# Kernel tuning notes

Hardware: AMD Instinct MI355X
Metric: run time of the kernel (lower is better)

The kernel has to match this reference:

```python
import jax, jax.numpy as jnp
import numpy as np

EPS = 1e-5
K = 5          # kernel size from SE3Convolution(5, ...)
STRIDE = 2
PAD = 3
C_HID = 52     # 4*dim(repr3x3=9) + dim(repr7=7) + dim(repr9=9)
N_CLASSES = 10


def conv3d(x, w):
    # x: [N, Cin, D, H, W], w: [Cout, Cin, K, K, K]
    return jax.lax.conv_general_dilated(
        x, w,
        window_strides=(STRIDE, STRIDE, STRIDE),
        padding=[(PAD, PAD)] * 3,
        dimension_numbers=("NCDHW", "OIDHW", "NCDHW"),
    )


def bn3d(x):
    # training-mode batch norm over (batch, spatial), per channel, no affine
    mean = jnp.mean(x, axis=(0, 2, 3, 4), keepdims=True)
    var = jnp.var(x, axis=(0, 2, 3, 4), keepdims=True)
    return (x - mean) * jax.lax.rsqrt(var + EPS)


def setup_inputs() -> dict:
    key = jax.random.key(0)
    ks = jax.random.split(key, 10)
    x = jax.random.normal(ks[0], (32, 1, 64, 64, 64), dtype=jnp.float32)
    s = 0.05
    w0 = jax.random.normal(ks[1], (C_HID, 1, K, K, K), jnp.float32) * s
    b0 = jax.random.normal(ks[2], (C_HID,), jnp.float32) * s
    w1 = jax.random.normal(ks[3], (C_HID, C_HID, K, K, K), jnp.float32) * s
    b1 = jax.random.normal(ks[4], (C_HID,), jnp.float32) * s
    w2 = jax.random.normal(ks[5], (C_HID, C_HID, K, K, K), jnp.float32) * s
    b2 = jax.random.normal(ks[6], (C_HID,), jnp.float32) * s
    w3 = jax.random.normal(ks[7], (N_CLASSES, C_HID, K, K, K), jnp.float32) * s
    gamma = jnp.ones((N_CLASSES,), jnp.float32)
    beta = jnp.zeros((N_CLASSES,), jnp.float32)
    return {"x": x, "w0": w0, "b0": b0, "w1": w1, "b1": b1,
            "w2": w2, "b2": b2, "w3": w3, "gamma": gamma, "beta": beta}


def reference(x, w0, b0, w1, b1, w2, b2, w3, gamma, beta):
    # bn_in: BatchNorm3d(1, affine=False)
    h = bn3d(x)
    # three conv blocks with scalar batch norm + bias + ReLU (non_lin layers)
    for w, b in ((w0, b0), (w1, b1), (w2, b2)):
        h = conv3d(h, w)
        h = bn3d(h)
        h = jax.nn.relu(h + b[None, :, None, None, None])
    # final conv (no nonlinearity)
    h = conv3d(h, w3)
    # global average pool over x, y, z -> [batch, classes]
    h = jnp.mean(h, axis=(2, 3, 4))
    # bn_out: affine batch norm over the batch dim, per class
    mean = jnp.mean(h, axis=0, keepdims=True)
    var = jnp.var(h, axis=0, keepdims=True)
    h = (h - mean) * jax.lax.rsqrt(var + EPS)
    return h * gamma[None, :] + beta[None, :]
```

## Files before the change

### kernel.cpp

```cpp
#include <hip/hip_runtime.h>
#include <hip/hip_bf16.h>

#define EPSV 1e-5f
constexpr int NB = 32;

typedef short bf16x8 __attribute__((ext_vector_type(8)));
typedef short short4v __attribute__((ext_vector_type(4)));
typedef float f32x4 __attribute__((ext_vector_type(4)));

__device__ inline float bf2f(short s) {
  return __uint_as_float(((unsigned)(unsigned short)s) << 16);
}
__device__ inline short f2bf(float f) {
  unsigned u = __float_as_uint(f);
  unsigned r = (u + 0x7FFFu + ((u >> 16) & 1u)) >> 16;
  return (short)r;
}

__global__ __launch_bounds__(256) void reduce_partial_f32(
    const float* __restrict__ in, int spatial, float* __restrict__ part,
    int totb, int boff)
{
  const int b = blockIdx.x;
  const int nblk = gridDim.x;
  float s = 0.f, s2 = 0.f;
  for (int n = 0; n < NB; ++n) {
    const float* p = in + (size_t)n * spatial;
    for (int i = b * 256 + threadIdx.x; i < spatial; i += nblk * 256) {
      float v = p[i];
      s += v; s2 += v * v;
    }
  }
  __shared__ float sh[256], sh2[256];
  int tid = threadIdx.x;
  sh[tid] = s; sh2[tid] = s2;
  __syncthreads();
  for (int off = 128; off > 0; off >>= 1) {
    if (tid < off) { sh[tid] += sh[tid + off]; sh2[tid] += sh2[tid + off]; }
    __syncthreads();
  }
  if (tid == 0) {
    part[(size_t)(boff + b) * 2 + 0] = sh[0];
    part[(size_t)(boff + b) * 2 + 1] = sh2[0];
  }
}

__global__ __launch_bounds__(256) void reduce_cl(
    const short* __restrict__ y, long nrows,
    float* __restrict__ part, int totb, int boff)
{
  const int b = blockIdx.x, nblk = gridDim.x;
  const int c = threadIdx.x & 63, seg = threadIdx.x >> 6;
  float s = 0.f, s2 = 0.f;
  for (long r = (long)b * 4 + seg; r < nrows; r += (long)nblk * 4) {
    float v = bf2f(y[r * 64 + c]);
    s += v; s2 += v * v;
  }
  __shared__ float sh[4][64], sh2[4][64];
  sh[seg][c] = s; sh2[seg][c] = s2;
  __syncthreads();
  if (seg == 0) {
    float a = sh[0][c] + sh[1][c] + sh[2][c] + sh[3][c];
    float a2 = sh2[0][c] + sh2[1][c] + sh2[2][c] + sh2[3][c];
    part[((size_t)c * totb + boff + b) * 2 + 0] = a;
    part[((size_t)c * totb + boff + b) * 2 + 1] = a2;
  }
}

__global__ __launch_bounds__(64) void reduce_final(
    const float* __restrict__ part, int nblk, int C, float* __restrict__ sums)
{
  const int c = blockIdx.x;
  float s = 0.f, s2 = 0.f;
  for (int b = threadIdx.x; b < nblk; b += 64) {
    s  += part[((size_t)c * nblk + b) * 2 + 0];
    s2 += part[((size_t)c * nblk + b) * 2 + 1];
  }
  for (int off = 32; off > 0; off >>= 1) {
    s  += __shfl_down(s, off);
    s2 += __shfl_down(s2, off);
  }
  if (threadIdx.x == 0) { sums[c] = s; sums[C + c] = s2; }
}

__global__ __launch_bounds__(64) void aff_k(
    const float* __restrict__ st, const float* __restrict__ bias,
    float cnt_inv, int creal, float* __restrict__ a, float* __restrict__ c)
{
  int t = threadIdx.x;
  float mean = st[t] * cnt_inv;
  float var  = st[64 + t] * cnt_inv - mean * mean;
  float inv  = rsqrtf(var + EPSV);
  bool ok = t < creal;
  a[t] = ok ? inv : 0.f;
  c[t] = ok ? (-mean * inv + bias[t]) : 0.f;
}

__global__ __launch_bounds__(256) void repack_k(
    const float* __restrict__ w, short* __restrict__ wt,
    int CO, int CIN, int COP)
{
  long total = 125L * COP * 64;
  for (long idx = (long)blockIdx.x * 256 + threadIdx.x; idx < total;
       idx += (long)gridDim.x * 256) {
    int tap = (int)(idx / (COP * 64));
    int r   = (int)(idx % (COP * 64));
    int co = r >> 6, ci = r & 63;
    float v = (co < CO && ci < CIN) ? w[((size_t)co * CIN + ci) * 125 + tap] : 0.f;
    wt[idx] = f2bf(v);
  }
}

__global__ __launch_bounds__(256) void repack_w0(
    const float* __restrict__ w, short* __restrict__ wt)
{
  for (int idx = blockIdx.x * 256 + threadIdx.x; idx < 64 * 128;
       idx += gridDim.x * 256) {
    int co = idx >> 7, k = idx & 127;
    float v = (co < 52 && k < 125) ? w[co * 125 + k] : 0.f;
    wt[idx] = f2bf(v);
  }
}

__global__ __launch_bounds__(256) void conv0_mfma(
    const float* __restrict__ x, const short* __restrict__ w0t,
    const float* __restrict__ stats, short* __restrict__ out,
    int n_in0, int n_out0)
{
  constexpr int IN = 64, OUT = 33;
  constexpr float CNTI = 1.0f / ((float)NB * IN * IN * IN);
  __shared__ __align__(16) char slab[64 * 256];

  const int tid = threadIdx.x;
  const int wv = tid >> 6, ln = tid & 63;
  const int cs = ln >> 4;
  const int ntile0 = blockIdx.x * 64;
  const int od = blockIdx.y;
  const int img = blockIdx.z;

  const float mean = stats[0] * CNTI;
  const float inv  = rsqrtf(stats[1] * CNTI - mean * mean + EPSV);

  bf16x8 afr[4];
  {
    const short* wrow = w0t + (wv * 16 + (ln & 15)) * 128 + cs * 8;
    #pragma unroll
    for (int ks = 0; ks < 4; ++ks) afr[ks] = *(const bf16x8*)(wrow + ks * 32);
  }

  const float* xi = x + (size_t)(n_in0 + img) * (IN * IN * IN);
  const int id_base = 2 * od - 3;
  for (int u = tid; u < 1024; u += 256) {
    const int nl = u >> 4, s = u & 15;
    const int ng = ntile0 + nl;
    const int oh = ng / OUT, ow = ng - oh * OUT;
    const bool nok = ng < OUT * OUT;
    const int ih_base = 2 * oh - 3, iw_base = 2 * ow - 3;
    bf16x8 pk;
    #pragma unroll
    for (int e = 0; e < 8; ++e) {
      const int k = s * 8 + e;
      float f = 0.f;
      if (nok && k < 125) {
        const int kd = k / 25, r = k - kd * 25;
        const int kh = r / 5, kw = r - kh * 5;
        const int id = id_base + kd, ih = ih_base + kh, iw = iw_base + kw;
        if ((unsigned)id < (unsigned)IN && (unsigned)ih < (unsigned)IN &&
            (unsigned)iw < (unsigned)IN)
          f = (xi[((size_t)id * IN + ih) * IN + iw] - mean) * inv;
      }
      pk[e] = f2bf(f);
    }
    const int slot = (s & 8) | ((s & 7) ^ (nl & 7));
    *(bf16x8*)(slab + nl * 256 + slot * 16) = pk;
  }
  __syncthreads();

  const int nl = ln & 15;
  #pragma unroll
  for (int nt = 0; nt < 4; ++nt) {
    f32x4 acc = (f32x4){0.f, 0.f, 0.f, 0.f};
    const int nn = nt * 16 + nl;
    #pragma unroll
    for (int ks = 0; ks < 4; ++ks) {
      const int s = ks * 4 + cs;
      const int slot = (s & 8) | ((s & 7) ^ (nn & 7));
      bf16x8 b = *(const bf16x8*)(slab + nn * 256 + slot * 16);
      acc = __builtin_amdgcn_mfma_f32_16x16x32_bf16(afr[ks], b, acc, 0, 0, 0);
    }
    const int ng = ntile0 + nn;
    if (ng < OUT * OUT) {
      const int oh = ng / OUT, ow = ng - oh * OUT;
      short4v pk;
      #pragma unroll
      for (int r = 0; r < 4; ++r) pk[r] = f2bf(acc[r]);
      size_t base = ((((size_t)(n_out0 + img) * OUT + od) * OUT + oh) * OUT + ow) * 64;
      *(short4v*)(out + base + wv * 16 + cs * 4) = pk;
    }
  }
}

__device__ inline int swz(int lin, int cs) {
  int row = lin >> 1;
  int slot = (((lin & 1) << 2) | cs) ^ (row & 7);
  return row * 128 + slot * 16;
}

template<int IN, int OUT, int OHG>
__global__ __launch_bounds__(256) void conv_m4(
    const short* __restrict__ yin, const short* __restrict__ wt,
    const float* __restrict__ affa, const float* __restrict__ affc,
    short* __restrict__ yout, int n_out0)
{
  constexpr int W = 2 * OUT + 3;
  constexpr int H = 2 * OHG + 3;
  constexpr int LIN = H * W;
  constexpr int ROWS = (LIN + 1) / 2;
  constexpr int NT = (OHG * OUT + 15) / 16;
  constexpr int OHT = (OUT + OHG - 1) / OHG;
  constexpr int LINM = LIN - 1 - 4 * W - 4;

  __shared__ __align__(16) char slab[ROWS * 128];
  __shared__ float s_a[64], s_c[64];

  const int tid = threadIdx.x;
  const int wv = tid >> 6, ln = tid & 63;
  const int nl = ln & 15, cs = ln >> 4;

  int lin;
  if (gridDim.x & 7) lin = blockIdx.x;
  else {
    const int q = gridDim.x >> 3;
    lin = (blockIdx.x & 7) * q + (blockIdx.x >> 3);
  }
  const int oht = lin % OHT;
  const int t2  = lin / OHT;
  const int od  = t2 % OUT;
  const int nimg = t2 / OUT;
  const int oh0 = oht * OHG;

  if (tid < 64) { s_a[tid] = affa[tid]; s_c[tid] = affc[tid]; }

  int lb[NT]; bool vld[NT]; size_t obase[NT];
  #pragma unroll
  for (int nt = 0; nt < NT; ++nt) {
    int n = nt * 16 + nl;
    int ohl = n / OUT, ow = n - ohl * OUT;
    vld[nt] = (n < OHG * OUT) && (oh0 + ohl < OUT);
    int l = 2 * ohl * W + 2 * ow;
    lb[nt] = (l > LINM) ? LINM : l;
    obase[nt] = ((((size_t)(n_out0 + nimg) * OUT + od) * OUT + (oh0 + ohl)) * OUT + ow) * 64;
  }

  f32x4 acc[NT];
  #pragma unroll
  for (int nt = 0; nt < NT; ++nt) acc[nt] = (f32x4){0.f, 0.f, 0.f, 0.f};

  const int id_base = 2 * od - 3;
  const int ih_base = 2 * oh0 - 3;

  for (int ch = 0; ch < 2; ++ch) {
    for (int kd = 0; kd < 5; ++kd) {
      __syncthreads();
      {
        const int id = id_base + kd;
        const bool dok = (unsigned)id < (unsigned)IN;
        for (int u = tid; u < LIN * 4; u += 256) {
          int l = u >> 2, cs2 = u & 3;
          int hl = l / W, wl = l - hl * W;
          int ih = ih_base + hl;
          int iw = wl - 3;
          bf16x8 pk;
          if (dok && (unsigned)ih < (unsigned)IN && (unsigned)iw < (unsigned)IN) {
            size_t base = ((((size_t)nimg * IN + id) * IN + ih) * IN + iw) * 64
                          + ch * 32 + cs2 * 8;
            bf16x8 ld = *(const bf16x8*)(yin + base);
            #pragma unroll
            for (int e = 0; e < 8; ++e) {
              int c = ch * 32 + cs2 * 8 + e;
              pk[e] = f2bf(fmaxf(s_a[c] * bf2f(ld[e]) + s_c[c], 0.f));
            }
          } else {
            #pragma unroll
            for (int e = 0; e < 8; ++e) pk[e] = 0;
          }
          *(bf16x8*)(slab + swz(l, cs2)) = pk;
        }
      }
      __syncthreads();
      for (int kh = 0; kh < 5; ++kh) {
        const int tapb = (kd * 5 + kh) * 5;
        bf16x8 afr[5];
        #pragma unroll
        for (int kw = 0; kw < 5; ++kw)
          afr[kw] = *(const bf16x8*)(
              wt + ((size_t)(tapb + kw) * 64 + wv * 16 + nl) * 64 + ch * 32 + cs * 8);
        #pragma unroll
        for (int nt = 0; nt < NT; ++nt) {
          const int lin0 = lb[nt] + kh * W;
          #pragma unroll
          for (int kw = 0; kw < 5; ++kw) {
            bf16x8 b = *(const bf16x8*)(slab + swz(lin0 + kw, cs));
            acc[nt] = __builtin_amdgcn_mfma_f32_16x16x32_bf16(
                afr[kw], b, acc[nt], 0, 0, 0);
          }
        }
      }
    }
  }

  #pragma unroll
  for (int nt = 0; nt < NT; ++nt) {
    if (!vld[nt]) continue;
    short4v pk;
    #pragma unroll
    for (int r = 0; r < 4; ++r) pk[r] = f2bf(acc[nt][r]);
    *(short4v*)(yout + obase[nt] + wv * 16 + cs * 4) = pk;
  }
}

__global__ __launch_bounds__(256) void conv3_m(
    const short* __restrict__ yin, const short* __restrict__ wt,
    const float* __restrict__ affa, const float* __restrict__ affc,
    short* __restrict__ yout)
{
  constexpr int IN = 10, OUT = 6;
  constexpr int W = 15, LIN = 225, ROWS = 113;
  constexpr int LINM = LIN - 1 - 4 * W - 4;
  __shared__ __align__(16) char slab[ROWS * 128];
  __shared__ float s_a[64], s_c[64];

  const int tid = threadIdx.x, wv = tid >> 6, ln = tid & 63;
  const int nl = ln & 15, cs = ln >> 4;
  const int od = blockIdx.x, nimg = blockIdx.y;

  if (tid < 64) { s_a[tid] = affa[tid]; s_c[tid] = affc[tid]; }

  const int nn = wv * 16 + nl;
  const bool act = wv < 3;
  const bool vld = act && nn < 36;
  int ohl = nn / 6, ow = nn - ohl * 6;
  int lb = 2 * ohl * W + 2 * ow;
  if (lb > LINM) lb = LINM;
  const size_t obase = ((((size_t)nimg * 6 + od) * 6 + ohl) * 6 + ow) * 16;

  f32x4 acc = (f32x4){0.f, 0.f, 0.f, 0.f};
  const int id_base = 2 * od - 3;

  for (int ch = 0; ch < 2; ++ch) {
    for (int kd = 0; kd < 5; ++kd) {
      const int id = id_base + kd;
      const bool dok = (unsigned)id < (unsigned)IN;
      __syncthreads();
      for (int u = tid; u < 900; u += 256) {
        int l = u >> 2, cs2 = u & 3;
        int hl = l / 15, wl = l - hl * 15;
        int ih = hl - 3, iw = wl - 3;
        bf16x8 pk;
        if (dok && (unsigned)ih < (unsigned)IN && (unsigned)iw < (unsigned)IN) {
          bf16x8 ld = *(const bf16x8*)(yin + ((((size_t)nimg * IN + id) * IN + ih) * IN + iw) * 64
                                       + ch * 32 + cs2 * 8);
          #pragma unroll
          for (int e = 0; e < 8; ++e) {
            int c = ch * 32 + cs2 * 8 + e;
            pk[e] = f2bf(fmaxf(s_a[c] * bf2f(ld[e]) + s_c[c], 0.f));
          }
        } else {
          #pragma unroll
          for (int e = 0; e < 8; ++e) pk[e] = 0;
        }
        *(bf16x8*)(slab + swz(l, cs2)) = pk;
      }
      __syncthreads();
      if (act) {
        for (int kh = 0; kh < 5; ++kh) {
          const int tapb = (kd * 5 + kh) * 5;
          bf16x8 afr[5];
          #pragma unroll
          for (int kw = 0; kw < 5; ++kw)
            afr[kw] = *(const bf16x8*)(wt + ((size_t)(tapb + kw) * 16 + nl) * 64
                                       + ch * 32 + cs * 8);
          #pragma unroll
          for (int kw = 0; kw < 5; ++kw) {
            bf16x8 b = *(const bf16x8*)(slab + swz(lb + kh * W + kw, cs));
            acc = __builtin_amdgcn_mfma_f32_16x16x32_bf16(afr[kw], b, acc, 0, 0, 0);
          }
        }
      }
    }
  }
  if (vld) {
    short4v pk;
    #pragma unroll
    for (int r = 0; r < 4; ++r) pk[r] = f2bf(acc[r]);
    *(short4v*)(yout + obase + cs * 4) = pk;
  }
}

__global__ __launch_bounds__(320) void pool_bn(
    const short* __restrict__ y3, const float* __restrict__ gamma,
    const float* __restrict__ beta, float* __restrict__ out)
{
  __shared__ float pool[320];
  const int t = threadIdx.x;
  const int n = t / 10, c = t % 10;
  const short* p = y3 + (size_t)n * 216 * 16 + c;
  float s = 0.f;
  for (int i = 0; i < 216; ++i) s += bf2f(p[i * 16]);
  const float pv = s * (1.0f / 216.0f);
  pool[t] = pv;
  __syncthreads();
  float m = 0.f, m2 = 0.f;
  for (int nn = 0; nn < 32; ++nn) {
    float v = pool[nn * 10 + c];
    m += v; m2 += v * v;
  }
  m *= (1.0f / 32.0f);
  m2 = m2 * (1.0f / 32.0f) - m * m;
  out[t] = (pv - m) * rsqrtf(m2 + EPSV) * gamma[c] + beta[c];
}

extern "C" void kernel_launch(void* const* d_in, const int* in_sizes, int n_in,
                              void* d_out, int out_size, void* d_ws, size_t ws_size,
                              hipStream_t stream)
{
  const float* x  = (const float*)d_in[0];
  const float* w0 = (const float*)d_in[1];
  const float* b0 = (const float*)d_in[2];
  const float* w1 = (const float*)d_in[3];
  const float* b1 = (const float*)d_in[4];
  const float* w2 = (const float*)d_in[5];
  const float* b2 = (const float*)d_in[6];
  const float* w3 = (const float*)d_in[7];
  const float* gamma = (const float*)d_in[8];
  const float* beta  = (const float*)d_in[9];
  float* out = (float*)d_out;

  char* base = (char*)d_ws;
  size_t off = 0;
  auto alloc = [&](size_t bytes) -> void* {
    void* p = base + off;
    off = (off + bytes + 255) & ~(size_t)255;
    return p;
  };
  short* y1  = (short*)alloc((size_t)32 * 5832 * 64 * 2);
  short* y2  = (short*)alloc((size_t)32 * 1000 * 64 * 2);
  short* y3  = (short*)alloc((size_t)32 * 216 * 16 * 2);
  short* w1t = (short*)alloc((size_t)125 * 64 * 64 * 2);
  short* w2t = (short*)alloc((size_t)125 * 64 * 64 * 2);
  short* w3t = (short*)alloc((size_t)125 * 16 * 64 * 2);
  short* w0t = (short*)alloc((size_t)64 * 128 * 2);
  float* st_in = (float*)alloc(1024);
  float* st0 = (float*)alloc(1024);
  float* st1 = (float*)alloc(1024);
  float* st2 = (float*)alloc(1024);
  float* a0 = (float*)alloc(256); float* c0 = (float*)alloc(256);
  float* a1 = (float*)alloc(256); float* c1 = (float*)alloc(256);
  float* a2 = (float*)alloc(256); float* c2 = (float*)alloc(256);
  float* part = (float*)alloc(64 * 1024 * 2 * 4);
  short* y0 = (short*)(base + off);
  size_t rem = (ws_size > off + 256) ? (ws_size - off - 256) : 0;
  const size_t Y0_IMG = (size_t)35937 * 64;
  int CH;
  if      (rem >= Y0_IMG * 32 * 2) CH = 32;
  else if (rem >= Y0_IMG * 16 * 2) CH = 16;
  else if (rem >= Y0_IMG * 8 * 2)  CH = 8;
  else if (rem >= Y0_IMG * 4 * 2)  CH = 4;
  else if (rem >= Y0_IMG * 2 * 2)  CH = 2;
  else                             CH = 1;
  const int nch = 32 / CH;

  repack_k<<<512, 256, 0, stream>>>(w1, w1t, 52, 52, 64);
  repack_k<<<512, 256, 0, stream>>>(w2, w2t, 52, 52, 64);
  repack_k<<<256, 256, 0, stream>>>(w3, w3t, 10, 52, 16);
  repack_w0<<<32, 256, 0, stream>>>(w0, w0t);

  reduce_partial_f32<<<128, 256, 0, stream>>>(x, 64 * 64 * 64, part, 128, 0);
  reduce_final<<<1, 64, 0, stream>>>(part, 128, 1, st_in);

  const float cnt0 = 1.0f / ((float)NB * 35937.0f);
  const float cnt1 = 1.0f / ((float)NB * 5832.0f);
  const float cnt2 = 1.0f / ((float)NB * 1000.0f);

  if (CH == 32) {
    conv0_mfma<<<dim3(18, 33, 32), 256, 0, stream>>>(x, w0t, st_in, y0, 0, 0);
    reduce_cl<<<1024, 256, 0, stream>>>(y0, (long)32 * 35937, part, 1024, 0);
    reduce_final<<<64, 64, 0, stream>>>(part, 1024, 64, st0);
    aff_k<<<1, 64, 0, stream>>>(st0, b0, cnt0, 52, a0, c0);
    conv_m4<33, 18, 2><<<9 * 18 * 32, 256, 0, stream>>>(
        y0, w1t, a0, c0, y1, 0);
  } else {
    for (int ck = 0; ck < nch; ++ck) {
      conv0_mfma<<<dim3(18, 33, CH), 256, 0, stream>>>(x, w0t, st_in, y0, ck * CH, 0);
      reduce_cl<<<32, 256, 0, stream>>>(y0, (long)CH * 35937, part, nch * 32, ck * 32);
    }
    reduce_final<<<64, 64, 0, stream>>>(part, nch * 32, 64, st0);
    aff_k<<<1, 64, 0, stream>>>(st0, b0, cnt0, 52, a0, c0);
    for (int ck = 0; ck < nch; ++ck) {
      conv0_mfma<<<dim3(18, 33, CH), 256, 0, stream>>>(x, w0t, st_in, y0, ck * CH, 0);
      conv_m4<33, 18, 2><<<9 * 18 * CH, 256, 0, stream>>>(
          y0, w1t, a0, c0, y1, ck * CH);
    }
  }

  reduce_cl<<<256, 256, 0, stream>>>(y1, (long)32 * 5832, part, 256, 0);
  reduce_final<<<64, 64, 0, stream>>>(part, 256, 64, st1);
  aff_k<<<1, 64, 0, stream>>>(st1, b1, cnt1, 52, a1, c1);

  conv_m4<18, 10, 4><<<3 * 10 * 32, 256, 0, stream>>>(
      y1, w2t, a1, c1, y2, 0);

  reduce_cl<<<32, 256, 0, stream>>>(y2, (long)32 * 1000, part, 32, 0);
  reduce_final<<<64, 64, 0, stream>>>(part, 32, 64, st2);
  aff_k<<<1, 64, 0, stream>>>(st2, b2, cnt2, 52, a2, c2);

  conv3_m<<<dim3(6, 32), 256, 0, stream>>>(y2, w3t, a2, c2, y3);

  pool_bn<<<1, 320, 0, stream>>>(y3, gamma, beta, out);
}
```

Baseline: 1.304 ms.

## Prefetch next input slab into registers while computing current conv phase

Flattens the channel-half and depth-tap loops into ten phases and loads the next phase's global input slab into registers before the MFMA loop of the current phase, then applies the affine+ReLU transform and writes it to LDS at the start of the following phase. This is meant to hide global load latency behind the matrix-core work instead of stalling at each slab fill. It costs extra registers for the prefetch buffer, which may reduce occupancy.

```diff
diff --git a/kernel.cpp b/kernel.cpp
--- a/kernel.cpp
+++ b/kernel.cpp
@@ -219,6 +219,7 @@
   constexpr int NT = (OHG * OUT + 15) / 16;
   constexpr int OHT = (OUT + OHG - 1) / OHG;
   constexpr int LINM = LIN - 1 - 4 * W - 4;
+  constexpr int P = (LIN * 4 + 255) / 256;
 
   __shared__ __align__(16) char slab[ROWS * 128];
   __shared__ float s_a[64], s_c[64];
@@ -259,51 +260,89 @@
   const int id_base = 2 * od - 3;
   const int ih_base = 2 * oh0 - 3;
 
-  for (int ch = 0; ch < 2; ++ch) {
-    for (int kd = 0; kd < 5; ++kd) {
-      __syncthreads();
-      {
-        const int id = id_base + kd;
-        const bool dok = (unsigned)id < (unsigned)IN;
-        for (int u = tid; u < LIN * 4; u += 256) {
+  bf16x8 pf[P];
+  bool   pfb[P];
+  {
+    const int id = id_base + 0;
+    const bool dok = (unsigned)id < (unsigned)IN;
+    #pragma unroll
+    for (int p = 0; p < P; ++p) {
+      int u = tid + p * 256;
+      bool ok = false;
+      bf16x8 v = {0, 0, 0, 0, 0, 0, 0, 0};
+      if (u < LIN * 4) {
+        int l = u >> 2, cs2 = u & 3;
+        int hl = l / W, wl = l - hl * W;
+        int ih = ih_base + hl, iw = wl - 3;
+        ok = dok && (unsigned)ih < (unsigned)IN && (unsigned)iw < (unsigned)IN;
+        if (ok)
+          v = *(const bf16x8*)(yin + ((((size_t)nimg * IN + id) * IN + ih) * IN + iw) * 64
+                               + cs2 * 8);
+      }
+      pf[p] = v; pfb[p] = ok;
+    }
+  }
+
+  #pragma unroll 1
+  for (int ph = 0; ph < 10; ++ph) {
+    const int ch = ph / 5;
+    const int kd = ph - ch * 5;
+    __syncthreads();
+    #pragma unroll
+    for (int p = 0; p < P; ++p) {
+      int u = tid + p * 256;
+      if (u < LIN * 4) {
+        int l = u >> 2, cs2 = u & 3;
+        bf16x8 pk = {0, 0, 0, 0, 0, 0, 0, 0};
+        if (pfb[p]) {
+          #pragma unroll
+          for (int e = 0; e < 8; ++e) {
+            int c = ch * 32 + cs2 * 8 + e;
+            pk[e] = f2bf(fmaxf(s_a[c] * bf2f(pf[p][e]) + s_c[c], 0.f));
+          }
+        }
+        *(bf16x8*)(slab + swz(l, cs2)) = pk;
+      }
+    }
+    if (ph < 9) {
+      const int ch2 = (ph + 1) / 5;
+      const int kd2 = (ph + 1) - ch2 * 5;
+      const int id = id_base + kd2;
+      const bool dok = (unsigned)id < (unsigned)IN;
+      #pragma unroll
+      for (int p = 0; p < P; ++p) {
+        int u = tid + p * 256;
+        bool ok = false;
+        bf16x8 v = {0, 0, 0, 0, 0, 0, 0, 0};
+        if (u < LIN * 4) {
           int l = u >> 2, cs2 = u & 3;
           int hl = l / W, wl = l - hl * W;
-          int ih = ih_base + hl;
-          int iw = wl - 3;
-          bf16x8 pk;
-          if (dok && (unsigned)ih < (unsigned)IN && (unsigned)iw < (unsigned)IN) {
-            size_t base = ((((size_t)nimg * IN + id) * IN + ih) * IN + iw) * 64
-                          + ch * 32 + cs2 * 8;
-            bf16x8 ld = *(const bf16x8*)(yin + base);
-            #pragma unroll
-            for (int e = 0; e < 8; ++e) {
-              int c = ch * 32 + cs2 * 8 + e;
-              pk[e] = f2bf(fmaxf(s_a[c] * bf2f(ld[e]) + s_c[c], 0.f));
-            }
-          } else {
-            #pragma unroll
-            for (int e = 0; e < 8; ++e) pk[e] = 0;
-          }
-          *(bf16x8*)(slab + swz(l, cs2)) = pk;
+          int ih = ih_base + hl, iw = wl - 3;
+          ok = dok && (unsigned)ih < (unsigned)IN && (unsigned)iw < (unsigned)IN;
+          if (ok)
+            v = *(const bf16x8*)(yin + ((((size_t)nimg * IN + id) * IN + ih) * IN + iw) * 64
+                                 + ch2 * 32 + cs2 * 8);
         }
-      }
-      __syncthreads();
-      for (int kh = 0; kh < 5; ++kh) {
-        const int tapb = (kd * 5 + kh) * 5;
-        bf16x8 afr[5];
+        pf[p] = v; pfb[p] = ok;
+      }
+      __builtin_amdgcn_sched_barrier(0);
+    }
+    __syncthreads();
+    for (int kh = 0; kh < 5; ++kh) {
+      const int tapb = (kd * 5 + kh) * 5;
+      bf16x8 afr[5];
+      #pragma unroll
+      for (int kw = 0; kw < 5; ++kw)
+        afr[kw] = *(const bf16x8*)(
+            wt + ((size_t)(tapb + kw) * 64 + wv * 16 + nl) * 64 + ch * 32 + cs * 8);
+      #pragma unroll
+      for (int nt = 0; nt < NT; ++nt) {
+        const int lin0 = lb[nt] + kh * W;
         #pragma unroll
-        for (int kw = 0; kw < 5; ++kw)
-          afr[kw] = *(const bf16x8*)(
-              wt + ((size_t)(tapb + kw) * 64 + wv * 16 + nl) * 64 + ch * 32 + cs * 8);
-        #pragma unroll
-        for (int nt = 0; nt < NT; ++nt) {
-          const int lin0 = lb[nt] + kh * W;
-          #pragma unroll
-          for (int kw = 0; kw < 5; ++kw) {
-            bf16x8 b = *(const bf16x8*)(slab + swz(lin0 + kw, cs));
-            acc[nt] = __builtin_amdgcn_mfma_f32_16x16x32_bf16(
-                afr[kw], b, acc[nt], 0, 0, 0);
-          }
+        for (int kw = 0; kw < 5; ++kw) {
+          bf16x8 b = *(const bf16x8*)(slab + swz(lin0 + kw, cs));
+          acc[nt] = __builtin_amdgcn_mfma_f32_16x16x32_bf16(
+              afr[kw], b, acc[nt], 0, 0, 0);
         }
       }
     }
```

Result: slower. 1.351 ms (+3.6%).
